# Optimization experiments

Hardware: AMD Instinct MI355X
Metric: run time of the kernel (lower is better)

The kernel has to match this reference:

```python
import jax, jax.numpy as jnp
import numpy as np

N_RAYS = 8192
N_SAMPLES = 128
HIDDEN = 128
SH_DIM = 16
RAY_EXT_FACTOR = 10.0


def rsh_cart_3(d):
    # Real spherical harmonics up to degree 3, Cartesian form (16 coeffs).
    x, y, z = d[..., 0], d[..., 1], d[..., 2]
    x2, y2, z2 = x * x, y * y, z * z
    xy, yz, xz = x * y, y * z, x * z
    return jnp.stack([
        0.282094791773878 * jnp.ones_like(x),
        -0.48860251190292 * y,
        0.48860251190292 * z,
        -0.48860251190292 * x,
        1.0925484305920792 * xy,
        -1.0925484305920792 * yz,
        0.94617469575756 * z2 - 0.31539156525252,
        -1.0925484305920792 * xz,
        0.5462742152960396 * (x2 - y2),
        0.5900435899266435 * y * (-3.0 * x2 + y2),
        2.8906114426405538 * xy * z,
        0.4570457994644658 * y * (1.0 - 5.0 * z2),
        0.3731763325901154 * z * (5.0 * z2 - 3.0),
        0.4570457994644658 * x * (1.0 - 5.0 * z2),
        1.445305721320277 * z * (x2 - y2),
        0.5900435899266435 * x * (-x2 + 3.0 * y2),
    ], axis=-1)


def setup_inputs() -> dict:
    key = jax.random.key(0)
    ks = jax.random.split(key, 11)
    o = jax.random.normal(ks[0], (N_RAYS, 3), dtype=jnp.float32)
    origins = 2.5 * o / jnp.linalg.norm(o, axis=-1, keepdims=True)
    # aim roughly at the unit AABB so most rays are active
    dirs = -origins + 0.2 * jax.random.normal(ks[1], (N_RAYS, 3), dtype=jnp.float32)
    u = jax.random.uniform(ks[2], (N_RAYS, N_SAMPLES), dtype=jnp.float32)
    s1 = 1.0 / np.sqrt(3.0)
    s2 = 1.0 / np.sqrt(HIDDEN)
    s3 = 1.0 / np.sqrt(HIDDEN + SH_DIM)
    return {
        'origins': origins,
        'dirs': dirs,
        'u': u,
        'W1': s1 * jax.random.normal(ks[3], (3, HIDDEN), dtype=jnp.float32),
        'b1': jnp.zeros((HIDDEN,), jnp.float32),
        'W2': s2 * jax.random.normal(ks[4], (HIDDEN, HIDDEN), dtype=jnp.float32),
        'b2': jnp.zeros((HIDDEN,), jnp.float32),
        'Wd': s2 * jax.random.normal(ks[5], (HIDDEN, 1), dtype=jnp.float32),
        'bd': jnp.zeros((1,), jnp.float32),
        'Wc': s3 * jax.random.normal(ks[6], (HIDDEN + SH_DIM, 3), dtype=jnp.float32),
        'bc': jnp.zeros((3,), jnp.float32),
    }


def reference(origins, dirs, u, W1, b1, W2, b2, Wd, bd, Wc, bc):
    B, T = u.shape
    # ---- AABB ([-1,1]^3) slab intersection -> tnear/tfar, active mask ----
    inv_d = 1.0 / dirs
    t1 = (-1.0 - origins) * inv_d
    t2 = (1.0 - origins) * inv_d
    tnear = jnp.maximum(jnp.max(jnp.minimum(t1, t2), axis=-1), 0.0)  # (B,)
    tfar = jnp.min(jnp.maximum(t1, t2), axis=-1)                      # (B,)
    active = tfar > tnear                                             # (B,)
    tfar_c = jnp.maximum(tfar, tnear + 1e-3)
    # ---- stratified ray step sampling ----
    frac = (jnp.arange(T, dtype=u.dtype) + u) / T                     # (B,T)
    ts = tnear[:, None] + (tfar_c - tnear)[:, None] * frac            # (B,T)
    xyz = origins[:, None, :] + dirs[:, None, :] * ts[..., None]      # (B,T,3)
    # aabb is [-1,1]^3 so ndc == xyz; spatial filter = bounds test
    xyz_ndc = xyz
    mask = jnp.all(jnp.abs(xyz_ndc) <= 1.0, axis=-1) & active[:, None]  # (B,T)
    dnorm = jnp.linalg.norm(dirs, axis=-1)                            # (B,)
    ynm = rsh_cart_3(dirs / dnorm[:, None])                           # (B,16)
    # ---- radiance field MLP over all sample points ----
    x = xyz_ndc.reshape(B * T, 3)
    h = jax.nn.relu(x @ W1 + b1)
    h = jax.nn.relu(h @ W2 + b2)
    sigma = jax.nn.softplus(h @ Wd + bd).reshape(B, T)
    cond = jnp.broadcast_to(ynm[:, None, :], (B, T, SH_DIM)).reshape(B * T, SH_DIM)
    color = jax.nn.sigmoid(jnp.concatenate([h, cond], axis=-1) @ Wc + bc).reshape(B, T, 3)
    # zero out points rejected by the spatial filter (torch writes only masked)
    sigma = sigma * mask
    color = color * mask[..., None]
    # ---- transmittance integration (integrate_timesteps) ----
    tfinal = tfar_c * RAY_EXT_FACTOR
    deltas = jnp.diff(ts, axis=-1, append=tfinal[:, None])            # (B,T)
    sd = sigma * deltas * dnorm[:, None]
    csum = jnp.cumsum(sd, axis=-1)
    # weights_i = T_i * alpha_i = exp(-csum_{i-1}) - exp(-csum_i)
    weights = jnp.exp(sd - csum) - jnp.exp(-csum)                     # (B,T)
    color_out = jnp.einsum('bt,btc->bc', weights, color)              # (B,3)
    alpha_out = jnp.sum(weights, axis=-1, keepdims=True)              # (B,1)
    rgba = jnp.concatenate([color_out, alpha_out], axis=-1)           # (B,4)
    return jnp.where(active[:, None], rgba, 0.0)
```

## Files before the change

kernel.cpp:

```cpp
#include <hip/hip_runtime.h>
#include <math.h>

#define NRAYS 8192
#define T 128
#define H 128
#define SHD 16
#define RPB 2
#define NBLK (NRAYS / RPB)

using short8 = __attribute__((ext_vector_type(8))) short;
using f32x4  = __attribute__((ext_vector_type(4))) float;

__device__ __forceinline__ float softplus_f(float x) {
  return fmaxf(x, 0.f) + log1pf(expf(-fabsf(x)));
}

__device__ __forceinline__ unsigned f2bf(float f) {
  unsigned u = __float_as_uint(f);
  return (u + 0x7fffu + ((u >> 16) & 1u)) >> 16;
}

__device__ __forceinline__ unsigned pkbf(float a, float b) {
  const unsigned ua = __float_as_uint(a) + 0x8000u;
  const unsigned ub = __float_as_uint(b) + 0x8000u;
  return __builtin_amdgcn_perm(ub, ua, 0x07060302u);
}

__global__ void preprocess(const float* __restrict__ W2, const float* __restrict__ Wd,
                           const float* __restrict__ Wc,
                           unsigned short* __restrict__ w2t,
                           unsigned short* __restrict__ woutf) {
  const int t = blockIdx.x * 256 + threadIdx.x;
  if (t < 16384) {
    const int n = t >> 7, p = t & 127;
    const int o = (p >> 3) ^ (n & 7);
    const int k = o * 8 + (p & 7);
    w2t[t] = (unsigned short)f2bf(W2[k * 128 + n]);
  }
  if (t < 2048) {
    const int kk = t >> 9, L = (t >> 3) & 63, j = t & 7;
    const int c = L & 15, g = L >> 4;
    const int k = kk * 32 + g * 8 + j;
    float v = 0.f;
    if (c == 0) v = Wd[k];
    else if (c < 4) v = Wc[k * 3 + (c - 1)];
    woutf[t] = (unsigned short)f2bf(v);
  }
}

__global__ __launch_bounds__(256, 2) void nerf_render(
    const float* __restrict__ origins, const float* __restrict__ dirs,
    const float* __restrict__ u, const float* __restrict__ W1,
    const float* __restrict__ b1, const float* __restrict__ b2,
    const float* __restrict__ bd, const float* __restrict__ Wc,
    const float* __restrict__ bc, const unsigned short* __restrict__ w2t,
    const unsigned short* __restrict__ woutf, float* __restrict__ out)
{
  const int ray0 = blockIdx.x * RPB;
  const int tid = threadIdx.x;
  const int L = tid & 63;
  const int w = tid >> 6;
  const int g = L >> 4;
  const int c = L & 15;

  __shared__ __align__(16) short Bs[16384];
  __shared__ __align__(16) short Wouts[2048];
  __shared__ __align__(16) short As2[4 * 640];
  __shared__ __align__(16) float2 bsl[RPB * H];
  __shared__ float ts_s[RPB * T];
  __shared__ float mask_s[RPB * T];
  __shared__ float rayp[RPB][8];
  __shared__ float wred[4][4];
  __shared__ float wtot[4];

  {
    const float4* src = (const float4*)w2t;
    float4* dst = (float4*)Bs;
    #pragma unroll
    for (int i = 0; i < 8; ++i) dst[tid + i * 256] = src[tid + i * 256];
    ((float4*)Wouts)[tid] = ((const float4*)woutf)[tid];
  }

  {
    const int r = tid >> 7, tl = tid & 127;
    const int gr = ray0 + r;
    const float ox = origins[gr*3+0], oy = origins[gr*3+1], oz = origins[gr*3+2];
    const float dx = dirs[gr*3+0],  dy = dirs[gr*3+1],  dz = dirs[gr*3+2];
    const float ix = 1.f/dx, iy = 1.f/dy, iz = 1.f/dz;
    const float t1x = (-1.f-ox)*ix, t2x = (1.f-ox)*ix;
    const float t1y = (-1.f-oy)*iy, t2y = (1.f-oy)*iy;
    const float t1z = (-1.f-oz)*iz, t2z = (1.f-oz)*iz;
    float tnear = fmaxf(fmaxf(fminf(t1x,t2x), fminf(t1y,t2y)), fminf(t1z,t2z));
    tnear = fmaxf(tnear, 0.f);
    const float tfar = fminf(fminf(fmaxf(t1x,t2x), fmaxf(t1y,t2y)), fmaxf(t1z,t2z));
    const bool  active = tfar > tnear;
    const float tfar_c = fmaxf(tfar, tnear + 1e-3f);
    const float ut = u[gr*T + tl];
    const float frac = ((float)tl + ut) * (1.f/(float)T);
    const float tt = tnear + (tfar_c - tnear) * frac;
    const float px = fmaf(dx, tt, ox);
    const float py = fmaf(dy, tt, oy);
    const float pz = fmaf(dz, tt, oz);
    ts_s[tid] = tt;
    const bool m = (fabsf(px) <= 1.f) && (fabsf(py) <= 1.f) && (fabsf(pz) <= 1.f) && active;
    mask_s[tid] = m ? 1.f : 0.f;
    const float w0 = W1[tl], w1v = W1[H + tl], w2v = W1[2*H + tl];
    bsl[r*H + tl] = make_float2(
        fmaf(ox, w0, fmaf(oy, w1v, fmaf(oz, w2v, b1[tl]))),
        fmaf(dx, w0, fmaf(dy, w1v, dz * w2v)));
    if (tl == 0) {
      rayp[r][0] = tfar_c;
      rayp[r][1] = sqrtf(dx*dx + dy*dy + dz*dz);
      rayp[r][2] = active ? 1.f : 0.f;
    }
  }
  if (tid < RPB) {
    const int gr = ray0 + tid;
    const float dx = dirs[gr*3+0], dy = dirs[gr*3+1], dz = dirs[gr*3+2];
    const float dnorm = sqrtf(dx*dx + dy*dy + dz*dz);
    const float nx = dx/dnorm, ny = dy/dnorm, nz = dz/dnorm;
    const float x2 = nx*nx, y2 = ny*ny, z2 = nz*nz;
    const float xy = nx*ny, yz = ny*nz, xz = nx*nz;
    float ynm[16];
    ynm[0]  = 0.282094791773878f;
    ynm[1]  = -0.48860251190292f*ny;
    ynm[2]  = 0.48860251190292f*nz;
    ynm[3]  = -0.48860251190292f*nx;
    ynm[4]  = 1.0925484305920792f*xy;
    ynm[5]  = -1.0925484305920792f*yz;
    ynm[6]  = 0.94617469575756f*z2 - 0.31539156525252f;
    ynm[7]  = -1.0925484305920792f*xz;
    ynm[8]  = 0.5462742152960396f*(x2-y2);
    ynm[9]  = 0.5900435899266435f*ny*(-3.f*x2+y2);
    ynm[10] = 2.8906114426405538f*xy*nz;
    ynm[11] = 0.4570457994644658f*ny*(1.f-5.f*z2);
    ynm[12] = 0.3731763325901154f*nz*(5.f*z2-3.f);
    ynm[13] = 0.4570457994644658f*nx*(1.f-5.f*z2);
    ynm[14] = 1.445305721320277f*nz*(x2-y2);
    ynm[15] = 0.5900435899266435f*nx*(-x2+3.f*y2);
    float cp0 = bc[0], cp1 = bc[1], cp2 = bc[2];
    #pragma unroll
    for (int s = 0; s < SHD; ++s) {
      cp0 = fmaf(ynm[s], Wc[(H+s)*3+0], cp0);
      cp1 = fmaf(ynm[s], Wc[(H+s)*3+1], cp1);
      cp2 = fmaf(ynm[s], Wc[(H+s)*3+2], cp2);
    }
    rayp[tid][3] = cp0; rayp[tid][4] = cp1; rayp[tid][5] = cp2;
  }
  __syncthreads();

  f32x4 acc[4][8];
  #pragma unroll
  for (int mt = 0; mt < 8; ++mt) {
    const float4 bv = *(const float4*)&b2[mt*16 + g*4];
    #pragma unroll
    for (int tm = 0; tm < 4; ++tm) {
      acc[tm][mt][0] = bv.x; acc[tm][mt][1] = bv.y;
      acc[tm][mt][2] = bv.z; acc[tm][mt][3] = bv.w;
    }
  }

  const int rayw = w >> 1;
  const float t0 = ts_s[64*w + c];
  const float t1 = ts_s[64*w + 16 + c];
  const float t2 = ts_s[64*w + 32 + c];
  const float t3 = ts_s[64*w + 48 + c];
  const float2* bslr = bsl + rayw * H;

  #pragma unroll
  for (int ks = 0; ks < 4; ++ks) {
    const int kb = ks*32 + g*8;
    float ha[8], hb_[8], hc[8], hd[8];
    #pragma unroll
    for (int j = 0; j < 8; ++j) {
      const float2 p = bslr[kb + j];
      ha[j]  = fmaxf(fmaf(t0, p.y, p.x), 0.f);
      hb_[j] = fmaxf(fmaf(t1, p.y, p.x), 0.f);
      hc[j]  = fmaxf(fmaf(t2, p.y, p.x), 0.f);
      hd[j]  = fmaxf(fmaf(t3, p.y, p.x), 0.f);
    }
    union U { uint4 u; short8 s; } A0, A1, A2, A3;
    A0.u = make_uint4(pkbf(ha[0],ha[1]),  pkbf(ha[2],ha[3]),  pkbf(ha[4],ha[5]),  pkbf(ha[6],ha[7]));
    A1.u = make_uint4(pkbf(hb_[0],hb_[1]),pkbf(hb_[2],hb_[3]),pkbf(hb_[4],hb_[5]),pkbf(hb_[6],hb_[7]));
    A2.u = make_uint4(pkbf(hc[0],hc[1]),  pkbf(hc[2],hc[3]),  pkbf(hc[4],hc[5]),  pkbf(hc[6],hc[7]));
    A3.u = make_uint4(pkbf(hd[0],hd[1]),  pkbf(hd[2],hd[3]),  pkbf(hd[4],hd[5]),  pkbf(hd[6],hd[7]));
    const int swb = ((ks*4 + g) ^ (c & 7)) * 8;
    #pragma unroll
    for (int mt = 0; mt < 8; ++mt) {
      const short8 wf = *(const short8*)&Bs[(mt*16 + c)*128 + swb];
      acc[0][mt] = __builtin_amdgcn_mfma_f32_16x16x32_bf16(wf, A0.s, acc[0][mt], 0, 0, 0);
      acc[1][mt] = __builtin_amdgcn_mfma_f32_16x16x32_bf16(wf, A1.s, acc[1][mt], 0, 0, 0);
      acc[2][mt] = __builtin_amdgcn_mfma_f32_16x16x32_bf16(wf, A2.s, acc[2][mt], 0, 0, 0);
      acc[3][mt] = __builtin_amdgcn_mfma_f32_16x16x32_bf16(wf, A3.s, acc[3][mt], 0, 0, 0);
    }
  }

  __syncthreads();
  float4* SredP = (float4*)Bs;

  short* As2w = As2 + w * 640;
  short8 wa[4];
  #pragma unroll
  for (int kk = 0; kk < 4; ++kk)
    wa[kk] = *(const short8*)&Wouts[(kk*64 + L)*8];

  #pragma unroll
  for (int tm = 0; tm < 4; ++tm) {
    f32x4 oacc;
    oacc[0] = 0.f; oacc[1] = 0.f; oacc[2] = 0.f; oacc[3] = 0.f;
    #pragma unroll
    for (int kk = 0; kk < 4; ++kk) {
      #pragma unroll
      for (int i = 0; i < 2; ++i) {
        const f32x4 a = acc[tm][kk*2 + i];
        const float h0 = fmaxf(a[0], 0.f);
        const float h1 = fmaxf(a[1], 0.f);
        const float h2 = fmaxf(a[2], 0.f);
        const float h3 = fmaxf(a[3], 0.f);
        *(uint2*)&As2w[c*40 + i*16 + g*4] = make_uint2(pkbf(h0, h1), pkbf(h2, h3));
      }
      const short8 hbf = *(const short8*)&As2w[c*40 + g*8];
      oacc = __builtin_amdgcn_mfma_f32_16x16x32_bf16(wa[kk], hbf, oacc, 0, 0, 0);
    }
    if (g == 0)
      SredP[64*w + 16*tm + c] = make_float4(oacc[0], oacc[1], oacc[2], oacc[3]);
  }
  __syncthreads();

  const int r2 = tid >> 7, tl2 = tid & 127;
  const float tfar_c2 = rayp[r2][0];
  const float dnorm2  = rayp[r2][1];
  const float4 sv = SredP[tid];
  const float mk = mask_s[tid];
  const float sigma = softplus_f(sv.x + bd[0]) * mk;
  const float cp0 = sv.y + rayp[r2][3];
  const float cp1 = sv.z + rayp[r2][4];
  const float cp2 = sv.w + rayp[r2][5];
  const float cc0 = mk / (1.f + expf(-cp0));
  const float cc1 = mk / (1.f + expf(-cp1));
  const float cc2 = mk / (1.f + expf(-cp2));
  const float tt = ts_s[tid];
  const float tnext = (tl2 < T-1) ? ts_s[tid + 1] : tfar_c2 * 10.f;
  const float sd = sigma * (tnext - tt) * dnorm2;

  float val = sd;
  #pragma unroll
  for (int off = 1; off < 64; off <<= 1) {
    const float tmp = __shfl_up(val, off);
    if (L >= off) val += tmp;
  }
  if (L == 63) wtot[w] = val;
  __syncthreads();
  const float csum = val + ((w & 1) ? wtot[w - 1] : 0.f);

  float wgt = expf(sd - csum) - expf(-csum);
  float wcx = wgt * cc0, wcy = wgt * cc1, wcz = wgt * cc2;
  #pragma unroll
  for (int mm = 32; mm >= 1; mm >>= 1) {
    wgt += __shfl_xor(wgt, mm);
    wcx += __shfl_xor(wcx, mm);
    wcy += __shfl_xor(wcy, mm);
    wcz += __shfl_xor(wcz, mm);
  }
  if (L == 0) { wred[w][0] = wgt; wred[w][1] = wcx; wred[w][2] = wcy; wred[w][3] = wcz; }
  __syncthreads();
  if (tid < RPB) {
    const int rr = tid;
    const float aw = wred[2*rr][0] + wred[2*rr+1][0];
    const float o0 = wred[2*rr][1] + wred[2*rr+1][1];
    const float o1 = wred[2*rr][2] + wred[2*rr+1][2];
    const float o2 = wred[2*rr][3] + wred[2*rr+1][3];
    const bool act = rayp[rr][2] != 0.f;
    out[(ray0+rr)*4+0] = act ? o0 : 0.f;
    out[(ray0+rr)*4+1] = act ? o1 : 0.f;
    out[(ray0+rr)*4+2] = act ? o2 : 0.f;
    out[(ray0+rr)*4+3] = act ? aw : 0.f;
  }
}

extern "C" void kernel_launch(void* const* d_in, const int* in_sizes, int n_in,
                              void* d_out, int out_size, void* d_ws, size_t ws_size,
                              hipStream_t stream) {
  const float* origins = (const float*)d_in[0];
  const float* dirs    = (const float*)d_in[1];
  const float* u       = (const float*)d_in[2];
  const float* W1      = (const float*)d_in[3];
  const float* b1      = (const float*)d_in[4];
  const float* W2      = (const float*)d_in[5];
  const float* b2      = (const float*)d_in[6];
  const float* Wd      = (const float*)d_in[7];
  const float* bd      = (const float*)d_in[8];
  const float* Wc      = (const float*)d_in[9];
  const float* bc      = (const float*)d_in[10];

  unsigned short* w2t   = (unsigned short*)d_ws;
  unsigned short* woutf = (unsigned short*)((char*)d_ws + 32768);

  preprocess<<<64, 256, 0, stream>>>(W2, Wd, Wc, w2t, woutf);
  nerf_render<<<NBLK, 256, 0, stream>>>(origins, dirs, u, W1, b1, b2, bd, Wc, bc,
                                        w2t, woutf, (float*)d_out);
}
```

Baseline: 143.3 us.

## Process one ray per block and load output weights directly to registers

```diff
diff --git a/kernel.cpp b/kernel.cpp
--- a/kernel.cpp
+++ b/kernel.cpp
@@ -5,8 +5,6 @@
 #define T 128
 #define H 128
 #define SHD 16
-#define RPB 2
-#define NBLK (NRAYS / RPB)
 
 using short8 = __attribute__((ext_vector_type(8))) short;
 using f32x4  = __attribute__((ext_vector_type(4))) float;
@@ -48,7 +46,7 @@
   }
 }
 
-__global__ __launch_bounds__(256, 2) void nerf_render(
+__global__ __launch_bounds__(256, 3) void nerf_render(
     const float* __restrict__ origins, const float* __restrict__ dirs,
     const float* __restrict__ u, const float* __restrict__ W1,
     const float* __restrict__ b1, const float* __restrict__ b2,
@@ -56,7 +54,7 @@
     const float* __restrict__ bc, const unsigned short* __restrict__ w2t,
     const unsigned short* __restrict__ woutf, float* __restrict__ out)
 {
-  const int ray0 = blockIdx.x * RPB;
+  const int ray = blockIdx.x;
   const int tid = threadIdx.x;
   const int L = tid & 63;
   const int w = tid >> 6;
@@ -64,28 +62,26 @@
   const int c = L & 15;
 
   __shared__ __align__(16) short Bs[16384];
-  __shared__ __align__(16) short Wouts[2048];
   __shared__ __align__(16) short As2[4 * 640];
-  __shared__ __align__(16) float2 bsl[RPB * H];
-  __shared__ float ts_s[RPB * T];
-  __shared__ float mask_s[RPB * T];
-  __shared__ float rayp[RPB][8];
-  __shared__ float wred[4][4];
-  __shared__ float wtot[4];
+  __shared__ __align__(16) float2 bsl[H];
+  __shared__ float ts_s[T];
+  __shared__ float mask_s[T];
+  __shared__ __align__(16) float4 SredP[T];
+  __shared__ float rayp[8];
+  __shared__ float wred[2][4];
+  __shared__ float wtot[2];
 
   {
     const float4* src = (const float4*)w2t;
     float4* dst = (float4*)Bs;
     #pragma unroll
     for (int i = 0; i < 8; ++i) dst[tid + i * 256] = src[tid + i * 256];
-    ((float4*)Wouts)[tid] = ((const float4*)woutf)[tid];
-  }
-
-  {
-    const int r = tid >> 7, tl = tid & 127;
-    const int gr = ray0 + r;
-    const float ox = origins[gr*3+0], oy = origins[gr*3+1], oz = origins[gr*3+2];
-    const float dx = dirs[gr*3+0],  dy = dirs[gr*3+1],  dz = dirs[gr*3+2];
+  }
+
+  if (tid < T) {
+    const int tl = tid;
+    const float ox = origins[ray*3+0], oy = origins[ray*3+1], oz = origins[ray*3+2];
+    const float dx = dirs[ray*3+0],  dy = dirs[ray*3+1],  dz = dirs[ray*3+2];
     const float ix = 1.f/dx, iy = 1.f/dy, iz = 1.f/dz;
     const float t1x = (-1.f-ox)*ix, t2x = (1.f-ox)*ix;
     const float t1y = (-1.f-oy)*iy, t2y = (1.f-oy)*iy;
@@ -95,28 +91,26 @@
     const float tfar = fminf(fminf(fmaxf(t1x,t2x), fmaxf(t1y,t2y)), fmaxf(t1z,t2z));
     const bool  active = tfar > tnear;
     const float tfar_c = fmaxf(tfar, tnear + 1e-3f);
-    const float ut = u[gr*T + tl];
+    const float ut = u[ray*T + tl];
     const float frac = ((float)tl + ut) * (1.f/(float)T);
     const float tt = tnear + (tfar_c - tnear) * frac;
     const float px = fmaf(dx, tt, ox);
     const float py = fmaf(dy, tt, oy);
     const float pz = fmaf(dz, tt, oz);
-    ts_s[tid] = tt;
+    ts_s[tl] = tt;
     const bool m = (fabsf(px) <= 1.f) && (fabsf(py) <= 1.f) && (fabsf(pz) <= 1.f) && active;
-    mask_s[tid] = m ? 1.f : 0.f;
+    mask_s[tl] = m ? 1.f : 0.f;
     const float w0 = W1[tl], w1v = W1[H + tl], w2v = W1[2*H + tl];
-    bsl[r*H + tl] = make_float2(
+    bsl[tl] = make_float2(
         fmaf(ox, w0, fmaf(oy, w1v, fmaf(oz, w2v, b1[tl]))),
         fmaf(dx, w0, fmaf(dy, w1v, dz * w2v)));
     if (tl == 0) {
-      rayp[r][0] = tfar_c;
-      rayp[r][1] = sqrtf(dx*dx + dy*dy + dz*dz);
-      rayp[r][2] = active ? 1.f : 0.f;
-    }
-  }
-  if (tid < RPB) {
-    const int gr = ray0 + tid;
-    const float dx = dirs[gr*3+0], dy = dirs[gr*3+1], dz = dirs[gr*3+2];
+      rayp[0] = tfar_c;
+      rayp[1] = sqrtf(dx*dx + dy*dy + dz*dz);
+      rayp[2] = active ? 1.f : 0.f;
+    }
+  } else if (tid == 128) {
+    const float dx = dirs[ray*3+0], dy = dirs[ray*3+1], dz = dirs[ray*3+2];
     const float dnorm = sqrtf(dx*dx + dy*dy + dz*dz);
     const float nx = dx/dnorm, ny = dy/dnorm, nz = dz/dnorm;
     const float x2 = nx*nx, y2 = ny*ny, z2 = nz*nz;
@@ -145,67 +139,54 @@
       cp1 = fmaf(ynm[s], Wc[(H+s)*3+1], cp1);
       cp2 = fmaf(ynm[s], Wc[(H+s)*3+2], cp2);
     }
-    rayp[tid][3] = cp0; rayp[tid][4] = cp1; rayp[tid][5] = cp2;
-  }
-  __syncthreads();
-
-  f32x4 acc[4][8];
+    rayp[3] = cp0; rayp[4] = cp1; rayp[5] = cp2;
+  }
+
+  short8 wa[4];
+  #pragma unroll
+  for (int kk = 0; kk < 4; ++kk)
+    wa[kk] = *(const short8*)&woutf[(kk*64 + L)*8];
+
+  f32x4 acc[2][8];
   #pragma unroll
   for (int mt = 0; mt < 8; ++mt) {
     const float4 bv = *(const float4*)&b2[mt*16 + g*4];
     #pragma unroll
-    for (int tm = 0; tm < 4; ++tm) {
+    for (int tm = 0; tm < 2; ++tm) {
       acc[tm][mt][0] = bv.x; acc[tm][mt][1] = bv.y;
       acc[tm][mt][2] = bv.z; acc[tm][mt][3] = bv.w;
     }
   }
-
-  const int rayw = w >> 1;
-  const float t0 = ts_s[64*w + c];
-  const float t1 = ts_s[64*w + 16 + c];
-  const float t2 = ts_s[64*w + 32 + c];
-  const float t3 = ts_s[64*w + 48 + c];
-  const float2* bslr = bsl + rayw * H;
+  __syncthreads();
+
+  const float t0 = ts_s[32*w + c];
+  const float t1 = ts_s[32*w + 16 + c];
 
   #pragma unroll
   for (int ks = 0; ks < 4; ++ks) {
     const int kb = ks*32 + g*8;
-    float ha[8], hb_[8], hc[8], hd[8];
+    float ha[8], hb_[8];
     #pragma unroll
     for (int j = 0; j < 8; ++j) {
-      const float2 p = bslr[kb + j];
+      const float2 p = bsl[kb + j];
       ha[j]  = fmaxf(fmaf(t0, p.y, p.x), 0.f);
       hb_[j] = fmaxf(fmaf(t1, p.y, p.x), 0.f);
-      hc[j]  = fmaxf(fmaf(t2, p.y, p.x), 0.f);
-      hd[j]  = fmaxf(fmaf(t3, p.y, p.x), 0.f);
-    }
-    union U { uint4 u; short8 s; } A0, A1, A2, A3;
+    }
+    union U { uint4 u; short8 s; } A0, A1;
     A0.u = make_uint4(pkbf(ha[0],ha[1]),  pkbf(ha[2],ha[3]),  pkbf(ha[4],ha[5]),  pkbf(ha[6],ha[7]));
     A1.u = make_uint4(pkbf(hb_[0],hb_[1]),pkbf(hb_[2],hb_[3]),pkbf(hb_[4],hb_[5]),pkbf(hb_[6],hb_[7]));
-    A2.u = make_uint4(pkbf(hc[0],hc[1]),  pkbf(hc[2],hc[3]),  pkbf(hc[4],hc[5]),  pkbf(hc[6],hc[7]));
-    A3.u = make_uint4(pkbf(hd[0],hd[1]),  pkbf(hd[2],hd[3]),  pkbf(hd[4],hd[5]),  pkbf(hd[6],hd[7]));
     const int swb = ((ks*4 + g) ^ (c & 7)) * 8;
     #pragma unroll
     for (int mt = 0; mt < 8; ++mt) {
       const short8 wf = *(const short8*)&Bs[(mt*16 + c)*128 + swb];
       acc[0][mt] = __builtin_amdgcn_mfma_f32_16x16x32_bf16(wf, A0.s, acc[0][mt], 0, 0, 0);
       acc[1][mt] = __builtin_amdgcn_mfma_f32_16x16x32_bf16(wf, A1.s, acc[1][mt], 0, 0, 0);
-      acc[2][mt] = __builtin_amdgcn_mfma_f32_16x16x32_bf16(wf, A2.s, acc[2][mt], 0, 0, 0);
-      acc[3][mt] = __builtin_amdgcn_mfma_f32_16x16x32_bf16(wf, A3.s, acc[3][mt], 0, 0, 0);
-    }
-  }
-
-  __syncthreads();
-  float4* SredP = (float4*)Bs;
+    }
+  }
 
   short* As2w = As2 + w * 640;
-  short8 wa[4];
-  #pragma unroll
-  for (int kk = 0; kk < 4; ++kk)
-    wa[kk] = *(const short8*)&Wouts[(kk*64 + L)*8];
-
-  #pragma unroll
-  for (int tm = 0; tm < 4; ++tm) {
+  #pragma unroll
+  for (int tm = 0; tm < 2; ++tm) {
     f32x4 oacc;
     oacc[0] = 0.f; oacc[1] = 0.f; oacc[2] = 0.f; oacc[3] = 0.f;
     #pragma unroll
@@ -223,25 +204,25 @@
       oacc = __builtin_amdgcn_mfma_f32_16x16x32_bf16(wa[kk], hbf, oacc, 0, 0, 0);
     }
     if (g == 0)
-      SredP[64*w + 16*tm + c] = make_float4(oacc[0], oacc[1], oacc[2], oacc[3]);
-  }
-  __syncthreads();
-
-  const int r2 = tid >> 7, tl2 = tid & 127;
-  const float tfar_c2 = rayp[r2][0];
-  const float dnorm2  = rayp[r2][1];
-  const float4 sv = SredP[tid];
-  const float mk = mask_s[tid];
-  const float sigma = softplus_f(sv.x + bd[0]) * mk;
-  const float cp0 = sv.y + rayp[r2][3];
-  const float cp1 = sv.z + rayp[r2][4];
-  const float cp2 = sv.w + rayp[r2][5];
-  const float cc0 = mk / (1.f + expf(-cp0));
-  const float cc1 = mk / (1.f + expf(-cp1));
-  const float cc2 = mk / (1.f + expf(-cp2));
-  const float tt = ts_s[tid];
-  const float tnext = (tl2 < T-1) ? ts_s[tid + 1] : tfar_c2 * 10.f;
-  const float sd = sigma * (tnext - tt) * dnorm2;
+      SredP[32*w + 16*tm + c] = make_float4(oacc[0], oacc[1], oacc[2], oacc[3]);
+  }
+  __syncthreads();
+
+  float sd = 0.f, cc0 = 0.f, cc1 = 0.f, cc2 = 0.f;
+  if (tid < T) {
+    const float4 sv = SredP[tid];
+    const float mk = mask_s[tid];
+    const float sigma = softplus_f(sv.x + bd[0]) * mk;
+    const float cp0 = sv.y + rayp[3];
+    const float cp1 = sv.z + rayp[4];
+    const float cp2 = sv.w + rayp[5];
+    cc0 = mk / (1.f + expf(-cp0));
+    cc1 = mk / (1.f + expf(-cp1));
+    cc2 = mk / (1.f + expf(-cp2));
+    const float tt = ts_s[tid];
+    const float tnext = (tid < T-1) ? ts_s[tid + 1] : rayp[0] * 10.f;
+    sd = sigma * (tnext - tt) * rayp[1];
+  }
 
   float val = sd;
   #pragma unroll
@@ -249,12 +230,15 @@
     const float tmp = __shfl_up(val, off);
     if (L >= off) val += tmp;
   }
-  if (L == 63) wtot[w] = val;
-  __syncthreads();
-  const float csum = val + ((w & 1) ? wtot[w - 1] : 0.f);
-
-  float wgt = expf(sd - csum) - expf(-csum);
-  float wcx = wgt * cc0, wcy = wgt * cc1, wcz = wgt * cc2;
+  if (tid < T && L == 63) wtot[w] = val;
+  __syncthreads();
+  const float csum = val + ((w == 1) ? wtot[0] : 0.f);
+
+  float wgt = 0.f, wcx = 0.f, wcy = 0.f, wcz = 0.f;
+  if (tid < T) {
+    wgt = expf(sd - csum) - expf(-csum);
+    wcx = wgt * cc0; wcy = wgt * cc1; wcz = wgt * cc2;
+  }
   #pragma unroll
   for (int mm = 32; mm >= 1; mm >>= 1) {
     wgt += __shfl_xor(wgt, mm);
@@ -262,19 +246,20 @@
     wcy += __shfl_xor(wcy, mm);
     wcz += __shfl_xor(wcz, mm);
   }
-  if (L == 0) { wred[w][0] = wgt; wred[w][1] = wcx; wred[w][2] = wcy; wred[w][3] = wcz; }
-  __syncthreads();
-  if (tid < RPB) {
-    const int rr = tid;
-    const float aw = wred[2*rr][0] + wred[2*rr+1][0];
-    const float o0 = wred[2*rr][1] + wred[2*rr+1][1];
-    const float o1 = wred[2*rr][2] + wred[2*rr+1][2];
-    const float o2 = wred[2*rr][3] + wred[2*rr+1][3];
-    const bool act = rayp[rr][2] != 0.f;
-    out[(ray0+rr)*4+0] = act ? o0 : 0.f;
-    out[(ray0+rr)*4+1] = act ? o1 : 0.f;
-    out[(ray0+rr)*4+2] = act ? o2 : 0.f;
-    out[(ray0+rr)*4+3] = act ? aw : 0.f;
+  if (tid < T && L == 0) {
+    wred[w][0] = wgt; wred[w][1] = wcx; wred[w][2] = wcy; wred[w][3] = wcz;
+  }
+  __syncthreads();
+  if (tid == 0) {
+    const float aw = wred[0][0] + wred[1][0];
+    const float o0 = wred[0][1] + wred[1][1];
+    const float o1 = wred[0][2] + wred[1][2];
+    const float o2 = wred[0][3] + wred[1][3];
+    const bool act = rayp[2] != 0.f;
+    out[ray*4+0] = act ? o0 : 0.f;
+    out[ray*4+1] = act ? o1 : 0.f;
+    out[ray*4+2] = act ? o2 : 0.f;
+    out[ray*4+3] = act ? aw : 0.f;
   }
 }
 
@@ -297,6 +282,6 @@
   unsigned short* woutf = (unsigned short*)((char*)d_ws + 32768);
 
   preprocess<<<64, 256, 0, stream>>>(W2, Wd, Wc, w2t, woutf);
-  nerf_render<<<NBLK, 256, 0, stream>>>(origins, dirs, u, W1, b1, b2, bd, Wc, bc,
-                                        w2t, woutf, (float*)d_out);
-}
+  nerf_render<<<NRAYS, 256, 0, stream>>>(origins, dirs, u, W1, b1, b2, bd, Wc, bc,
+                                         w2t, woutf, (float*)d_out);
+}
```

Result: slower. 146.6 us (+2.3%).
